# Performance work log

Measured on AMD Instinct MI355X. Metric: run time of the kernel, lower is better.

The kernel has to match this reference:

```python
import jax, jax.numpy as jnp
import numpy as np

EMBED_DIM = 1024
NUM_HEADS = 16
HEAD_DIM = EMBED_DIM // NUM_HEADS
HIDDEN_DIM = 4096
EPS = 1e-5


def setup_inputs() -> dict:
    key = jax.random.key(0)
    ks = jax.random.split(key, 12)
    B, N, C, H = 4, 2048, EMBED_DIM, HIDDEN_DIM
    s = 0.02
    return {
        "x": jax.random.normal(ks[0], (B, N, C), jnp.float32),
        "ln1_g": jnp.ones((C,), jnp.float32),
        "ln1_b": jnp.zeros((C,), jnp.float32),
        "w_qkv": jax.random.normal(ks[1], (C, 3 * C), jnp.float32) * s,
        "w_proj": jax.random.normal(ks[2], (C, C), jnp.float32) * s,
        "b_proj": jnp.zeros((C,), jnp.float32),
        "ln2_g": jnp.ones((C,), jnp.float32),
        "ln2_b": jnp.zeros((C,), jnp.float32),
        "w1": jax.random.normal(ks[3], (C, H), jnp.float32) * s,
        "b1": jnp.zeros((H,), jnp.float32),
        "w2": jax.random.normal(ks[4], (H, C), jnp.float32) * s,
        "b2": jnp.zeros((C,), jnp.float32),
    }


def _layernorm(x, g, b):
    mu = jnp.mean(x, axis=-1, keepdims=True)
    var = jnp.mean(jnp.square(x - mu), axis=-1, keepdims=True)
    return (x - mu) * jax.lax.rsqrt(var + EPS) * g + b


def reference(x, ln1_g, ln1_b, w_qkv, w_proj, b_proj, ln2_g, ln2_b, w1, b1, w2, b2):
    B, N, C = x.shape
    # --- attention sub-block ---
    h = _layernorm(x, ln1_g, ln1_b)
    qkv = h @ w_qkv  # [B,N,3C]
    qkv = qkv.reshape(B, N, 3, NUM_HEADS, HEAD_DIM).transpose(2, 0, 3, 1, 4)
    q, k, v = qkv[0], qkv[1], qkv[2]  # each [B,H,N,D]
    scale = HEAD_DIM ** -0.5
    attn = jnp.einsum("bhqd,bhkd->bhqk", q, k) * scale  # materialized scores
    attn = jax.nn.softmax(attn, axis=-1)
    o = jnp.einsum("bhqk,bhkd->bhqd", attn, v)
    o = o.transpose(0, 2, 1, 3).reshape(B, N, C)
    x = x + (o @ w_proj + b_proj)
    # --- MLP sub-block ---
    h = _layernorm(x, ln2_g, ln2_b)
    h = jax.nn.gelu(h @ w1 + b1, approximate=False)
    x = x + (h @ w2 + b2)
    return x
```

## Files before the change

kernel.cpp:

```cpp
#include <hip/hip_runtime.h>

#define B_    4
#define SEQ   2048
#define CDIM  1024
#define NHEAD 16
#define HDIM  64
#define HID   4096
#define MTOK  (B_*SEQ)

typedef unsigned short ushort_t;
typedef __bf16 bf16x8 __attribute__((ext_vector_type(8)));
typedef float  floatx4 __attribute__((ext_vector_type(4)));
typedef short  sh4     __attribute__((ext_vector_type(4)));

static __device__ __forceinline__ float us2f(ushort_t u) {
    union { unsigned u; float f; } z; z.u = ((unsigned)u) << 16; return z.f;
}
static __device__ __forceinline__ ushort_t f2b(float f) {
    union { __bf16 h; ushort_t u; } z; z.h = (__bf16)f; return z.u;
}

static __device__ __forceinline__ floatx4 mfma16(sh4 a, sh4 b, floatx4 c) {
#if __has_builtin(__builtin_amdgcn_mfma_f32_16x16x16bf16_1k)
    return __builtin_amdgcn_mfma_f32_16x16x16bf16_1k(a, b, c, 0, 0, 0);
#else
    asm("v_mfma_f32_16x16x16_bf16 %0, %1, %2, %0" : "+v"(c) : "v"(a), "v"(b));
    return c;
#endif
}

static __device__ __forceinline__ void gl_lds16(const ushort_t* g, ushort_t* l) {
    __builtin_amdgcn_global_load_lds(
        (const __attribute__((address_space(1))) void*)g,
        (__attribute__((address_space(3))) void*)l,
        16, 0, 0);
}

__global__ void k_detect(const unsigned* __restrict__ g1, int* __restrict__ flagp) {
    if (threadIdx.x == 0) flagp[0] = (g1[0] == 0x3F803F80u) ? 0 : 1;
}

__global__ __launch_bounds__(256) void k_cvt_params(const int* __restrict__ flagp,
        const void* s0, const void* s1, const void* s2, const void* s3,
        const void* s4, const void* s5, const void* s6,
        ushort_t* __restrict__ dst) {
    const int flag = *flagp;
    const int seg = blockIdx.y;
    const int i = blockIdx.x * 256 + threadIdx.x;
    const int sizes[7] = {1024, 1024, 1024, 1024, 1024, 4096, 1024};
    const int offs[7]  = {0, 1024, 2048, 3072, 4096, 5120, 9216};
    const void* sp = seg == 0 ? s0 : seg == 1 ? s1 : seg == 2 ? s2 :
                     seg == 3 ? s3 : seg == 4 ? s4 : seg == 5 ? s5 : s6;
    if (i < sizes[seg]) {
        float v = flag ? ((const float*)sp)[i] : us2f(((const ushort_t*)sp)[i]);
        dst[offs[seg] + i] = f2b(v);
    }
}

__global__ __launch_bounds__(256) void k_transpose_all(const int* __restrict__ flagp,
        const void* s_qkv, const void* s_proj, const void* s_w1, const void* s_w2,
        ushort_t* __restrict__ d_qkv, ushort_t* __restrict__ d_proj,
        ushort_t* __restrict__ d_w1, ushort_t* __restrict__ d_w2) {
    const int id = blockIdx.x;
    const void* src; ushort_t* dst; int R, C, tile;
    if (id < 3072)      { src = s_qkv;  dst = d_qkv;  R = 1024; C = 3072; tile = id; }
    else if (id < 4096) { src = s_proj; dst = d_proj; R = 1024; C = 1024; tile = id - 3072; }
    else if (id < 8192) { src = s_w1;   dst = d_w1;   R = 1024; C = 4096; tile = id - 4096; }
    else                { src = s_w2;   dst = d_w2;   R = 4096; C = 1024; tile = id - 8192; }
    const int ct = C >> 5;
    const int c0 = (tile % ct) * 32, r0 = (tile / ct) * 32;
    const int flag = *flagp;
    __shared__ ushort_t tl[32][33];
    const int tx = threadIdx.x & 31, ty = threadIdx.x >> 5;
    #pragma unroll
    for (int i = ty; i < 32; i += 8) {
        const size_t gi = (size_t)(r0 + i) * C + c0 + tx;
        tl[i][tx] = flag ? f2b(((const float*)src)[gi]) : ((const ushort_t*)src)[gi];
    }
    __syncthreads();
    #pragma unroll
    for (int i = ty; i < 32; i += 8)
        dst[(size_t)(c0 + i) * R + r0 + tx] = tl[tx][i];
}

template <int SRC>
__global__ __launch_bounds__(256) void k_layernorm(const int* __restrict__ flagp,
                                                   const float* __restrict__ xf,
                                                   const ushort_t* __restrict__ xb,
                                                   const ushort_t* __restrict__ gam,
                                                   const ushort_t* __restrict__ bet,
                                                   ushort_t* __restrict__ out) {
    const int row = blockIdx.x, t = threadIdx.x;
    const int lane = t & 63, wv = t >> 6;
    const size_t base = (size_t)row * CDIM + t * 4;
    float v[4];
    if (SRC == 1 || *flagp != 0) {
        float4 f = *(const float4*)(xf + base);
        v[0] = f.x; v[1] = f.y; v[2] = f.z; v[3] = f.w;
    } else {
        ushort4 u = *(const ushort4*)(xb + base);
        v[0] = us2f(u.x); v[1] = us2f(u.y); v[2] = us2f(u.z); v[3] = us2f(u.w);
    }
    float s = v[0] + v[1] + v[2] + v[3];
    float s2 = v[0]*v[0] + v[1]*v[1] + v[2]*v[2] + v[3]*v[3];
    #pragma unroll
    for (int m = 1; m < 64; m <<= 1) {
        s  += __shfl_xor(s,  m, 64);
        s2 += __shfl_xor(s2, m, 64);
    }
    __shared__ float redbuf[8];
    if (lane == 0) { redbuf[wv] = s; redbuf[4 + wv] = s2; }
    __syncthreads();
    s  = redbuf[0] + redbuf[1] + redbuf[2] + redbuf[3];
    s2 = redbuf[4] + redbuf[5] + redbuf[6] + redbuf[7];
    const float mu  = s * (1.0f / CDIM);
    const float var = s2 * (1.0f / CDIM) - mu * mu;
    const float rstd = rsqrtf(var + 1e-5f);
    const int cb = t * 4;
    ushort4 o;
    o.x = f2b((v[0] - mu) * rstd * us2f(gam[cb + 0]) + us2f(bet[cb + 0]));
    o.y = f2b((v[1] - mu) * rstd * us2f(gam[cb + 1]) + us2f(bet[cb + 1]));
    o.z = f2b((v[2] - mu) * rstd * us2f(gam[cb + 2]) + us2f(bet[cb + 2]));
    o.w = f2b((v[3] - mu) * rstd * us2f(gam[cb + 3]) + us2f(bet[cb + 3]));
    *(ushort4*)(out + base) = o;
}

enum { EPI_QKV = 0, EPI_BIAS_RES_F32 = 1, EPI_BIAS_GELU_BF16 = 2, EPI_FINAL = 3 };

template <int EPI, int KDIM>
__global__ __launch_bounds__(512, 2) void k_gemm2(const ushort_t* __restrict__ A,
                                                  const ushort_t* __restrict__ Bt,
                                                  const ushort_t* __restrict__ bias,
                                                  const float* __restrict__ resF,
                                                  const ushort_t* __restrict__ resU,
                                                  float* __restrict__ outF,
                                                  ushort_t* __restrict__ outB,
                                                  ushort_t* __restrict__ outV,
                                                  const int* __restrict__ flagp,
                                                  int N) {
    constexpr int NT = KDIM / 64;
    __shared__ ushort_t As[3][256 * 64];
    __shared__ ushort_t Bs[3][128 * 64];
    const int t = threadIdx.x, lane = t & 63, wv = t >> 6;
    const int quad = lane >> 4, cc = lane & 15;
    const int wm = wv >> 2, wn = wv & 3;
    const int m0 = blockIdx.y * 256, n0 = blockIdx.x * 128;

    auto stage = [&](int kt, int bf) {
        const int k0 = kt * 64;
        #pragma unroll
        for (int i = 0; i < 4; i++) {
            const int L = i * 512 + t;
            const int row = L >> 3;
            const int kc = (L & 7) ^ (row & 7);
            gl_lds16(A + (size_t)(m0 + row) * KDIM + k0 + kc * 8,
                     As[bf] + (size_t)(i * 512 + wv * 64) * 8);
        }
        #pragma unroll
        for (int i = 0; i < 2; i++) {
            const int L = i * 512 + t;
            const int row = L >> 3;
            const int kc = (L & 7) ^ (row & 7);
            gl_lds16(Bt + (size_t)(n0 + row) * KDIM + k0 + kc * 8,
                     Bs[bf] + (size_t)(i * 512 + wv * 64) * 8);
        }
    };

    floatx4 zv = {0.f, 0.f, 0.f, 0.f};
    floatx4 acc[8][2];
    #pragma unroll
    for (int m = 0; m < 8; m++) { acc[m][0] = zv; acc[m][1] = zv; }

    stage(0, 0); stage(1, 1); stage(2, 2);
    asm volatile("s_waitcnt vmcnt(12)" ::: "memory");
    __builtin_amdgcn_s_barrier();

    int bt = 0;
    for (int kt = 0; kt < NT; ++kt) {
        const ushort_t* pAs = As[bt];
        const ushort_t* pBs = Bs[bt];
        bf16x8 af[8][2], bfr[2][2];
        #pragma unroll
        for (int ks = 0; ks < 2; ks++) {
            const int sl = ((ks * 4 + quad) ^ (cc & 7)) * 8;
            #pragma unroll
            for (int m = 0; m < 8; m++)
                af[m][ks] = *(const bf16x8*)(pAs + (size_t)(wm * 128 + m * 16 + cc) * 64 + sl);
            #pragma unroll
            for (int n = 0; n < 2; n++)
                bfr[n][ks] = *(const bf16x8*)(pBs + (size_t)(wn * 32 + n * 16 + cc) * 64 + sl);
        }
        __builtin_amdgcn_s_setprio(1);
        #pragma unroll
        for (int m = 0; m < 8; m++)
            #pragma unroll
            for (int n = 0; n < 2; n++)
                acc[m][n] = __builtin_amdgcn_mfma_f32_16x16x32_bf16(
                    af[m][0], bfr[n][0], acc[m][n], 0, 0, 0);
        __builtin_amdgcn_s_setprio(0);
        asm volatile("s_waitcnt lgkmcnt(0)" ::: "memory");
        __builtin_amdgcn_s_barrier();
        if (kt + 3 < NT) stage(kt + 3, bt);
        __builtin_amdgcn_s_setprio(1);
        #pragma unroll
        for (int m = 0; m < 8; m++)
            #pragma unroll
            for (int n = 0; n < 2; n++)
                acc[m][n] = __builtin_amdgcn_mfma_f32_16x16x32_bf16(
                    af[m][1], bfr[n][1], acc[m][n], 0, 0, 0);
        __builtin_amdgcn_s_setprio(0);
        if (kt + 3 < NT)      asm volatile("s_waitcnt vmcnt(12)" ::: "memory");
        else if (kt + 2 < NT) asm volatile("s_waitcnt vmcnt(6)" ::: "memory");
        else if (kt + 1 < NT) asm volatile("s_waitcnt vmcnt(0)" ::: "memory");
        __builtin_amdgcn_s_barrier();
        bt = (bt == 2) ? 0 : bt + 1;
    }

    int flag = 0;
    if (EPI == EPI_BIAS_RES_F32 || EPI == EPI_FINAL) flag = *flagp;

    #pragma unroll
    for (int m = 0; m < 8; m++) {
        #pragma unroll
        for (int n = 0; n < 2; n++) {
            const int col = n0 + wn * 32 + n * 16 + cc;
            if (EPI == EPI_QKV) {
                if (col < 2048) {
                    const float sc = (col < 1024) ? 0.125f * 1.44269504f : 1.0f;
                    #pragma unroll
                    for (int i = 0; i < 4; i++) {
                        const int row = m0 + wm * 128 + m * 16 + quad * 4 + i;
                        outB[(size_t)row * 3072 + col] = f2b(acc[m][n][i] * sc);
                    }
                } else {
                    const int hh = (col - 2048) >> 6, d = (col - 2048) & 63;
                    const int r0w = m0 + wm * 128 + m * 16 + quad * 4;
                    const int bh = (r0w >> 11) * NHEAD + hh;
                    const int np = r0w & (SEQ - 1);
                    ushort4 pk;
                    pk.x = f2b(acc[m][n][0]);
                    pk.y = f2b(acc[m][n][1]);
                    pk.z = f2b(acc[m][n][2]);
                    pk.w = f2b(acc[m][n][3]);
                    *(ushort4*)(outV + ((size_t)bh * 64 + d) * SEQ + np) = pk;
                }
            } else {
                const float bv = us2f(bias[col]);
                #pragma unroll
                for (int i = 0; i < 4; i++) {
                    const int row = m0 + wm * 128 + m * 16 + quad * 4 + i;
                    const size_t idx = (size_t)row * N + col;
                    float v = acc[m][n][i] + bv;
                    if (EPI == EPI_BIAS_RES_F32) {
                        outF[idx] = v + (flag ? resF[idx] : us2f(resU[idx]));
                    } else if (EPI == EPI_BIAS_GELU_BF16) {
                        float u = v * v;
                        float w = -2.3022134f * v * __builtin_fmaf(0.044715f, u, 1.0f);
                        float e = __builtin_amdgcn_exp2f(fminf(w, 126.0f));
                        outB[idx] = f2b(v * __builtin_amdgcn_rcpf(1.0f + e));
                    } else {
                        float w = v + resF[idx];
                        if (flag != 0) outF[idx] = w;
                        else           outB[idx] = f2b(w);
                    }
                }
            }
        }
    }
}

__global__ __launch_bounds__(256) void k_attention(const ushort_t* __restrict__ qkv,
                                                   const ushort_t* __restrict__ vT,
                                                   ushort_t* __restrict__ o) {
    __shared__ ushort_t Kc[2][64 * 64];
    __shared__ ushort_t Vt[2][64 * 64];

    const int bh = blockIdx.x, qt = blockIdx.y;
    const int b = bh >> 4, h = bh & 15;
    const int t = threadIdx.x, lane = t & 63, wv = t >> 6;
    const int quad = lane >> 4, cc = lane & 15;
    const size_t rstr = 3 * CDIM;
    const ushort_t* Qb = qkv + (size_t)b * SEQ * rstr + h * HDIM;
    const ushort_t* Kb = Qb + CDIM;
    const ushort_t* Vb = vT + (size_t)bh * HDIM * SEQ;

    bf16x8 aq[2][2];
    #pragma unroll
    for (int mt = 0; mt < 2; mt++) {
        const int qrow = qt * 128 + wv * 32 + mt * 16 + cc;
        aq[mt][0] = *(const bf16x8*)(Qb + (size_t)qrow * rstr + quad * 8);
        aq[mt][1] = *(const bf16x8*)(Qb + (size_t)qrow * rstr + 32 + quad * 8);
    }

    floatx4 zv = {0.f, 0.f, 0.f, 0.f};
    floatx4 oacc[2][4];
    floatx4 lv[2];
    #pragma unroll
    for (int mt = 0; mt < 2; mt++) {
        lv[mt] = zv;
        #pragma unroll
        for (int dg = 0; dg < 4; dg++) oacc[mt][dg] = zv;
    }
    const sh4 ones4 = {0x3F80, 0x3F80, 0x3F80, 0x3F80};

    auto stage = [&](int c, int buf) {
        const int k0 = c * 64;
        #pragma unroll
        for (int ii = 0; ii < 2; ii++) {
            const int L = ii * 256 + t;
            const int r = L >> 3;
            const int kc = (L & 7) ^ (r & 7);
            gl_lds16(Kb + (size_t)(k0 + r) * rstr + kc * 8,
                     &Kc[buf][(size_t)(ii * 256 + wv * 64) * 8]);
            gl_lds16(Vb + (size_t)r * SEQ + k0 + kc * 8,
                     &Vt[buf][(size_t)(ii * 256 + wv * 64) * 8]);
        }
    };

    stage(0, 0);

    for (int c = 0; c < SEQ / 64; c++) {
        __syncthreads();
        if (c + 1 < SEQ / 64) stage(c + 1, (c + 1) & 1);
        const int bf = c & 1;

        floatx4 s[2][4];
        #pragma unroll
        for (int mt = 0; mt < 2; mt++)
            #pragma unroll
            for (int g = 0; g < 4; g++) s[mt][g] = zv;
        #pragma unroll
        for (int g = 0; g < 4; g++) {
            const ushort_t* kr = &Kc[bf][(size_t)(g * 16 + cc) * 64];
            bf16x8 bk0 = *(const bf16x8*)(kr + (quad ^ (cc & 7)) * 8);
            bf16x8 bk1 = *(const bf16x8*)(kr + ((4 + quad) ^ (cc & 7)) * 8);
            #pragma unroll
            for (int mt = 0; mt < 2; mt++) {
                s[mt][g] = __builtin_amdgcn_mfma_f32_16x16x32_bf16(bk0, aq[mt][0], s[mt][g], 0, 0, 0);
                s[mt][g] = __builtin_amdgcn_mfma_f32_16x16x32_bf16(bk1, aq[mt][1], s[mt][g], 0, 0, 0);
            }
        }

        sh4 pb[2][4];
        #pragma unroll
        for (int mt = 0; mt < 2; mt++)
            #pragma unroll
            for (int g = 0; g < 4; g++)
                #pragma unroll
                for (int i = 0; i < 4; i++) {
                    float p = __builtin_amdgcn_exp2f(s[mt][g][i]);
                    union { __bf16 h; short u; } cv; cv.h = (__bf16)p;
                    pb[mt][g][i] = cv.u;
                }

        #pragma unroll
        for (int kg = 0; kg < 4; kg++) {
            #pragma unroll
            for (int mt = 0; mt < 2; mt++)
                lv[mt] = mfma16(ones4, pb[mt][kg], lv[mt]);
            #pragma unroll
            for (int dg = 0; dg < 4; dg++) {
                const int d = dg * 16 + cc;
                const int ph = ((kg * 2 + (quad >> 1)) ^ (d & 7)) * 8 + (quad & 1) * 4;
                sh4 va = *(const sh4*)(&Vt[bf][(size_t)d * 64 + ph]);
                #pragma unroll
                for (int mt = 0; mt < 2; mt++)
                    oacc[mt][dg] = mfma16(va, pb[mt][kg], oacc[mt][dg]);
            }
        }
    }

    #pragma unroll
    for (int mt = 0; mt < 2; mt++) {
        const float rl = __builtin_amdgcn_rcpf(lv[mt][0]);
        const int tok = b * SEQ + qt * 128 + wv * 32 + mt * 16 + cc;
        #pragma unroll
        for (int dg = 0; dg < 4; dg++) {
            ushort4 pk;
            pk.x = f2b(oacc[mt][dg][0] * rl);
            pk.y = f2b(oacc[mt][dg][1] * rl);
            pk.z = f2b(oacc[mt][dg][2] * rl);
            pk.w = f2b(oacc[mt][dg][3] * rl);
            *(ushort4*)(o + (size_t)tok * CDIM + h * HDIM + dg * 16 + quad * 4) = pk;
        }
    }
}

extern "C" void kernel_launch(void* const* d_in, const int* in_sizes, int n_in,
                              void* d_out, int out_size, void* d_ws, size_t ws_size,
                              hipStream_t stream) {
    const void* x     = d_in[0];
    const void* ln1g  = d_in[1];
    const void* ln1b  = d_in[2];
    const void* wqkv  = d_in[3];
    const void* wproj = d_in[4];
    const void* bproj = d_in[5];
    const void* ln2g  = d_in[6];
    const void* ln2b  = d_in[7];
    const void* w1    = d_in[8];
    const void* b1    = d_in[9];
    const void* w2    = d_in[10];
    const void* b2    = d_in[11];

    char* ws = (char*)d_ws;
    size_t off = 0;
    auto alloc = [&](size_t bytes) {
        void* p = ws + off;
        off += (bytes + 255) & ~(size_t)255;
        return p;
    };
    int*      flagp  = (int*)alloc(256);
    ushort_t* params = (ushort_t*)alloc((size_t)10240 * 2);
    ushort_t* wqkvT  = (ushort_t*)alloc((size_t)3072 * 1024 * 2);
    ushort_t* wprojT = (ushort_t*)alloc((size_t)1024 * 1024 * 2);
    ushort_t* w1T    = (ushort_t*)alloc((size_t)4096 * 1024 * 2);
    ushort_t* w2T    = (ushort_t*)alloc((size_t)1024 * 4096 * 2);
    ushort_t* vTb    = (ushort_t*)alloc((size_t)MTOK * CDIM * 2);
    float*    x1     = (float*)alloc((size_t)MTOK * CDIM * 4);
    ushort_t* bufA   = (ushort_t*)alloc((size_t)MTOK * HID * 2);
    ushort_t* bufB   = (ushort_t*)alloc((size_t)MTOK * 3 * CDIM * 2);

    ushort_t* p_ln1g = params + 0;
    ushort_t* p_ln1b = params + 1024;
    ushort_t* p_ln2g = params + 2048;
    ushort_t* p_ln2b = params + 3072;
    ushort_t* p_bprj = params + 4096;
    ushort_t* p_b1   = params + 5120;
    ushort_t* p_b2   = params + 9216;

    ushort_t* h   = bufA;
    ushort_t* qkv = bufB;
    ushort_t* oo  = bufA;
    ushort_t* h2  = bufB;
    ushort_t* hh  = bufA;

    k_detect<<<1, 64, 0, stream>>>((const unsigned*)ln1g, flagp);
    k_cvt_params<<<dim3(16, 7), 256, 0, stream>>>(flagp,
        ln1g, ln1b, ln2g, ln2b, bproj, b1, b2, params);
    k_transpose_all<<<12288, 256, 0, stream>>>(flagp,
        wqkv, wproj, w1, w2, wqkvT, wprojT, w1T, w2T);

    k_layernorm<0><<<MTOK, 256, 0, stream>>>(flagp, (const float*)x, (const ushort_t*)x, p_ln1g, p_ln1b, h);
    k_gemm2<EPI_QKV, 1024><<<dim3(24, 32), 512, 0, stream>>>(
        h, wqkvT, nullptr, nullptr, nullptr, nullptr, qkv, vTb, flagp, 3072);
    k_attention<<<dim3(B_ * NHEAD, SEQ / 128), 256, 0, stream>>>(qkv, vTb, oo);
    k_gemm2<EPI_BIAS_RES_F32, 1024><<<dim3(8, 32), 512, 0, stream>>>(
        oo, wprojT, p_bprj, (const float*)x, (const ushort_t*)x, x1, nullptr, nullptr, flagp, 1024);
    k_layernorm<1><<<MTOK, 256, 0, stream>>>(flagp, x1, nullptr, p_ln2g, p_ln2b, h2);
    k_gemm2<EPI_BIAS_GELU_BF16, 1024><<<dim3(32, 32), 512, 0, stream>>>(
        h2, w1T, p_b1, nullptr, nullptr, nullptr, hh, nullptr, flagp, 4096);
    k_gemm2<EPI_FINAL, 4096><<<dim3(8, 32), 512, 0, stream>>>(
        hh, w2T, p_b2, x1, nullptr, (float*)d_out, (ushort_t*)d_out, nullptr, flagp, 1024);
}
```

Measured before the change: 564.2 us.

## Retile GEMMs to 256-wide N tiles with double buffering and split LDS fragment loads

Replaces the 256x128 triple-buffered GEMM with a templated kernel using 256-wide N tiles and a configurable M tile (256 for QKV/FC1, 128 for proj/FC2), double-buffered in LDS. Each warp now computes FMx4 fragments, which raises MFMA reuse per LDS load. The second-half K fragments are loaded after the first MFMA batch instead of up front, so LDS reads overlap with compute. Grids are resized to match. Double buffering leaves less prefetch depth, and the 128-row config yields 256 blocks, which may underfill the CUs.

```diff
diff --git a/kernel.cpp b/kernel.cpp
--- a/kernel.cpp
+++ b/kernel.cpp
@@ -127,8 +127,8 @@
 
 enum { EPI_QKV = 0, EPI_BIAS_RES_F32 = 1, EPI_BIAS_GELU_BF16 = 2, EPI_FINAL = 3 };
 
-template <int EPI, int KDIM>
-__global__ __launch_bounds__(512, 2) void k_gemm2(const ushort_t* __restrict__ A,
+template <int EPI, int KDIM, int FM>
+__global__ __launch_bounds__(512, 2) void k_gemm3(const ushort_t* __restrict__ A,
                                                   const ushort_t* __restrict__ Bt,
                                                   const ushort_t* __restrict__ bias,
                                                   const float* __restrict__ resF,
@@ -138,18 +138,20 @@
                                                   ushort_t* __restrict__ outV,
                                                   const int* __restrict__ flagp,
                                                   int N) {
+    constexpr int BM = FM * 32;
+    constexpr int AR = BM / 64;
     constexpr int NT = KDIM / 64;
-    __shared__ ushort_t As[3][256 * 64];
-    __shared__ ushort_t Bs[3][128 * 64];
+    __shared__ ushort_t As[2][BM * 64];
+    __shared__ ushort_t Bs[2][256 * 64];
     const int t = threadIdx.x, lane = t & 63, wv = t >> 6;
     const int quad = lane >> 4, cc = lane & 15;
     const int wm = wv >> 2, wn = wv & 3;
-    const int m0 = blockIdx.y * 256, n0 = blockIdx.x * 128;
+    const int m0 = blockIdx.y * BM, n0 = blockIdx.x * 256;
 
     auto stage = [&](int kt, int bf) {
         const int k0 = kt * 64;
         #pragma unroll
-        for (int i = 0; i < 4; i++) {
+        for (int i = 0; i < AR; i++) {
             const int L = i * 512 + t;
             const int row = L >> 3;
             const int kc = (L & 7) ^ (row & 7);
@@ -157,7 +159,7 @@
                      As[bf] + (size_t)(i * 512 + wv * 64) * 8);
         }
         #pragma unroll
-        for (int i = 0; i < 2; i++) {
+        for (int i = 0; i < 4; i++) {
             const int L = i * 512 + t;
             const int row = L >> 3;
             const int kc = (L & 7) ^ (row & 7);
@@ -167,74 +169,86 @@
     };
 
     floatx4 zv = {0.f, 0.f, 0.f, 0.f};
-    floatx4 acc[8][2];
-    #pragma unroll
-    for (int m = 0; m < 8; m++) { acc[m][0] = zv; acc[m][1] = zv; }
-
-    stage(0, 0); stage(1, 1); stage(2, 2);
-    asm volatile("s_waitcnt vmcnt(12)" ::: "memory");
+    floatx4 acc[FM][4];
+    #pragma unroll
+    for (int m = 0; m < FM; m++)
+        #pragma unroll
+        for (int n = 0; n < 4; n++) acc[m][n] = zv;
+
+    stage(0, 0); stage(1, 1);
+    if constexpr (FM == 8) asm volatile("s_waitcnt vmcnt(8)" ::: "memory");
+    else                   asm volatile("s_waitcnt vmcnt(6)" ::: "memory");
     __builtin_amdgcn_s_barrier();
 
-    int bt = 0;
+    int cur = 0;
     for (int kt = 0; kt < NT; ++kt) {
-        const ushort_t* pAs = As[bt];
-        const ushort_t* pBs = Bs[bt];
-        bf16x8 af[8][2], bfr[2][2];
-        #pragma unroll
-        for (int ks = 0; ks < 2; ks++) {
-            const int sl = ((ks * 4 + quad) ^ (cc & 7)) * 8;
-            #pragma unroll
-            for (int m = 0; m < 8; m++)
-                af[m][ks] = *(const bf16x8*)(pAs + (size_t)(wm * 128 + m * 16 + cc) * 64 + sl);
-            #pragma unroll
-            for (int n = 0; n < 2; n++)
-                bfr[n][ks] = *(const bf16x8*)(pBs + (size_t)(wn * 32 + n * 16 + cc) * 64 + sl);
-        }
+        const ushort_t* pAs = As[cur];
+        const ushort_t* pBs = Bs[cur];
+        bf16x8 af[FM], bfr[4];
+        const int sl0 = (quad ^ (cc & 7)) * 8;
+        #pragma unroll
+        for (int m = 0; m < FM; m++)
+            af[m] = *(const bf16x8*)(pAs + (size_t)(wm * (FM * 16) + m * 16 + cc) * 64 + sl0);
+        #pragma unroll
+        for (int n = 0; n < 4; n++)
+            bfr[n] = *(const bf16x8*)(pBs + (size_t)(wn * 64 + n * 16 + cc) * 64 + sl0);
         __builtin_amdgcn_s_setprio(1);
         #pragma unroll
-        for (int m = 0; m < 8; m++)
-            #pragma unroll
-            for (int n = 0; n < 2; n++)
+        for (int m = 0; m < FM; m++)
+            #pragma unroll
+            for (int n = 0; n < 4; n++)
                 acc[m][n] = __builtin_amdgcn_mfma_f32_16x16x32_bf16(
-                    af[m][0], bfr[n][0], acc[m][n], 0, 0, 0);
+                    af[m], bfr[n], acc[m][n], 0, 0, 0);
         __builtin_amdgcn_s_setprio(0);
+        bf16x8 ag[FM], bg[4];
+        const int sl1 = ((4 + quad) ^ (cc & 7)) * 8;
+        #pragma unroll
+        for (int m = 0; m < FM; m++)
+            ag[m] = *(const bf16x8*)(pAs + (size_t)(wm * (FM * 16) + m * 16 + cc) * 64 + sl1);
+        #pragma unroll
+        for (int n = 0; n < 4; n++)
+            bg[n] = *(const bf16x8*)(pBs + (size_t)(wn * 64 + n * 16 + cc) * 64 + sl1);
         asm volatile("s_waitcnt lgkmcnt(0)" ::: "memory");
+        __builtin_amdgcn_sched_barrier(0);
         __builtin_amdgcn_s_barrier();
-        if (kt + 3 < NT) stage(kt + 3, bt);
+        if (kt + 2 < NT) stage(kt + 2, cur);
         __builtin_amdgcn_s_setprio(1);
         #pragma unroll
-        for (int m = 0; m < 8; m++)
-            #pragma unroll
-            for (int n = 0; n < 2; n++)
+        for (int m = 0; m < FM; m++)
+            #pragma unroll
+            for (int n = 0; n < 4; n++)
                 acc[m][n] = __builtin_amdgcn_mfma_f32_16x16x32_bf16(
-                    af[m][1], bfr[n][1], acc[m][n], 0, 0, 0);
+                    ag[m], bg[n], acc[m][n], 0, 0, 0);
         __builtin_amdgcn_s_setprio(0);
-        if (kt + 3 < NT)      asm volatile("s_waitcnt vmcnt(12)" ::: "memory");
-        else if (kt + 2 < NT) asm volatile("s_waitcnt vmcnt(6)" ::: "memory");
-        else if (kt + 1 < NT) asm volatile("s_waitcnt vmcnt(0)" ::: "memory");
+        if (kt + 2 < NT) {
+            if constexpr (FM == 8) asm volatile("s_waitcnt vmcnt(8)" ::: "memory");
+            else                   asm volatile("s_waitcnt vmcnt(6)" ::: "memory");
+        } else if (kt + 1 < NT) {
+            asm volatile("s_waitcnt vmcnt(0)" ::: "memory");
+        }
         __builtin_amdgcn_s_barrier();
-        bt = (bt == 2) ? 0 : bt + 1;
+        cur ^= 1;
     }
 
     int flag = 0;
     if (EPI == EPI_BIAS_RES_F32 || EPI == EPI_FINAL) flag = *flagp;
 
     #pragma unroll
-    for (int m = 0; m < 8; m++) {
-        #pragma unroll
-        for (int n = 0; n < 2; n++) {
-            const int col = n0 + wn * 32 + n * 16 + cc;
+    for (int m = 0; m < FM; m++) {
+        #pragma unroll
+        for (int n = 0; n < 4; n++) {
+            const int col = n0 + wn * 64 + n * 16 + cc;
             if (EPI == EPI_QKV) {
                 if (col < 2048) {
                     const float sc = (col < 1024) ? 0.125f * 1.44269504f : 1.0f;
                     #pragma unroll
                     for (int i = 0; i < 4; i++) {
-                        const int row = m0 + wm * 128 + m * 16 + quad * 4 + i;
+                        const int row = m0 + wm * (FM * 16) + m * 16 + quad * 4 + i;
                         outB[(size_t)row * 3072 + col] = f2b(acc[m][n][i] * sc);
                     }
                 } else {
                     const int hh = (col - 2048) >> 6, d = (col - 2048) & 63;
-                    const int r0w = m0 + wm * 128 + m * 16 + quad * 4;
+                    const int r0w = m0 + wm * (FM * 16) + m * 16 + quad * 4;
                     const int bh = (r0w >> 11) * NHEAD + hh;
                     const int np = r0w & (SEQ - 1);
                     ushort4 pk;
@@ -248,7 +262,7 @@
                 const float bv = us2f(bias[col]);
                 #pragma unroll
                 for (int i = 0; i < 4; i++) {
-                    const int row = m0 + wm * 128 + m * 16 + quad * 4 + i;
+                    const int row = m0 + wm * (FM * 16) + m * 16 + quad * 4 + i;
                     const size_t idx = (size_t)row * N + col;
                     float v = acc[m][n][i] + bv;
                     if (EPI == EPI_BIAS_RES_F32) {
@@ -441,14 +455,14 @@
         wqkv, wproj, w1, w2, wqkvT, wprojT, w1T, w2T);
 
     k_layernorm<0><<<MTOK, 256, 0, stream>>>(flagp, (const float*)x, (const ushort_t*)x, p_ln1g, p_ln1b, h);
-    k_gemm2<EPI_QKV, 1024><<<dim3(24, 32), 512, 0, stream>>>(
+    k_gemm3<EPI_QKV, 1024, 8><<<dim3(12, 32), 512, 0, stream>>>(
         h, wqkvT, nullptr, nullptr, nullptr, nullptr, qkv, vTb, flagp, 3072);
     k_attention<<<dim3(B_ * NHEAD, SEQ / 128), 256, 0, stream>>>(qkv, vTb, oo);
-    k_gemm2<EPI_BIAS_RES_F32, 1024><<<dim3(8, 32), 512, 0, stream>>>(
+    k_gemm3<EPI_BIAS_RES_F32, 1024, 4><<<dim3(4, 64), 512, 0, stream>>>(
         oo, wprojT, p_bprj, (const float*)x, (const ushort_t*)x, x1, nullptr, nullptr, flagp, 1024);
     k_layernorm<1><<<MTOK, 256, 0, stream>>>(flagp, x1, nullptr, p_ln2g, p_ln2b, h2);
-    k_gemm2<EPI_BIAS_GELU_BF16, 1024><<<dim3(32, 32), 512, 0, stream>>>(
+    k_gemm3<EPI_BIAS_GELU_BF16, 1024, 8><<<dim3(16, 32), 512, 0, stream>>>(
         h2, w1T, p_b1, nullptr, nullptr, nullptr, hh, nullptr, flagp, 4096);
-    k_gemm2<EPI_FINAL, 4096><<<dim3(8, 32), 512, 0, stream>>>(
+    k_gemm3<EPI_FINAL, 4096, 4><<<dim3(4, 64), 512, 0, stream>>>(
         hh, w2T, p_b2, x1, nullptr, (float*)d_out, (ushort_t*)d_out, nullptr, flagp, 1024);
 }
```

After: 534.7 us. 1.06x faster.

## Rewrite GEMM as templated 256-wide N tile with interleaved fragment loads

Applied to the files above, without the earlier changes.

Replaces the 256x128 GEMM tile with a templated BMx256 tile (BM 128 or 256), with double or triple buffering chosen by BM. The main loop is split into four phases that interleave LDS fragment loads with MFMA groups and issue the next global prefetch earlier, aiming to overlap LDS reads with matrix math. Each GEMM launch gets a new grid shape and BM choice. The extra barriers per k-step and the fewer blocks for the smaller GEMMs may cost synchronization overhead or reduce occupancy.

```diff
diff --git a/kernel.cpp b/kernel.cpp
--- a/kernel.cpp
+++ b/kernel.cpp
@@ -127,8 +127,8 @@
 
 enum { EPI_QKV = 0, EPI_BIAS_RES_F32 = 1, EPI_BIAS_GELU_BF16 = 2, EPI_FINAL = 3 };
 
-template <int EPI, int KDIM>
-__global__ __launch_bounds__(512, 2) void k_gemm2(const ushort_t* __restrict__ A,
+template <int EPI, int KDIM, int BM>
+__global__ __launch_bounds__(512, 2) void k_gemm4(const ushort_t* __restrict__ A,
                                                   const ushort_t* __restrict__ Bt,
                                                   const ushort_t* __restrict__ bias,
                                                   const float* __restrict__ resF,
@@ -138,103 +138,150 @@
                                                   ushort_t* __restrict__ outV,
                                                   const int* __restrict__ flagp,
                                                   int N) {
-    constexpr int NT = KDIM / 64;
-    __shared__ ushort_t As[3][256 * 64];
-    __shared__ ushort_t Bs[3][128 * 64];
+    constexpr int WR   = BM / 2;
+    constexpr int FR   = WR / 16;
+    constexpr int ART  = (BM * 64) / 4096;
+    constexpr int NT   = KDIM / 64;
+    constexpr int NBUF = (BM == 128) ? 3 : 2;
+    constexpr int LA   = NBUF - 1;
+    __shared__ ushort_t As[NBUF][BM * 64];
+    __shared__ ushort_t Bs[NBUF][256 * 64];
     const int t = threadIdx.x, lane = t & 63, wv = t >> 6;
     const int quad = lane >> 4, cc = lane & 15;
     const int wm = wv >> 2, wn = wv & 3;
-    const int m0 = blockIdx.y * 256, n0 = blockIdx.x * 128;
-
-    auto stage = [&](int kt, int bf) {
-        const int k0 = kt * 64;
-        #pragma unroll
-        for (int i = 0; i < 4; i++) {
-            const int L = i * 512 + t;
-            const int row = L >> 3;
-            const int kc = (L & 7) ^ (row & 7);
-            gl_lds16(A + (size_t)(m0 + row) * KDIM + k0 + kc * 8,
-                     As[bf] + (size_t)(i * 512 + wv * 64) * 8);
-        }
-        #pragma unroll
-        for (int i = 0; i < 2; i++) {
-            const int L = i * 512 + t;
-            const int row = L >> 3;
-            const int kc = (L & 7) ^ (row & 7);
-            gl_lds16(Bt + (size_t)(n0 + row) * KDIM + k0 + kc * 8,
-                     Bs[bf] + (size_t)(i * 512 + wv * 64) * 8);
+    const int m0 = blockIdx.y * BM, n0 = blockIdx.x * 256;
+
+    const int rl = lane >> 3, kc = (lane & 7) ^ (rl & 7);
+    auto stage_tile = [&](int kt, int d) {
+        #pragma unroll
+        for (int r = 0; r < ART; ++r) {
+            const int row = r * 64 + wv * 8 + rl;
+            gl_lds16(A + (size_t)(m0 + row) * KDIM + kt * 64 + kc * 8,
+                     As[d] + r * 4096 + wv * 512);
+        }
+        #pragma unroll
+        for (int r = 0; r < 4; ++r) {
+            const int row = r * 64 + wv * 8 + rl;
+            gl_lds16(Bt + (size_t)(n0 + row) * KDIM + kt * 64 + kc * 8,
+                     Bs[d] + r * 4096 + wv * 512);
         }
     };
 
     floatx4 zv = {0.f, 0.f, 0.f, 0.f};
-    floatx4 acc[8][2];
-    #pragma unroll
-    for (int m = 0; m < 8; m++) { acc[m][0] = zv; acc[m][1] = zv; }
-
-    stage(0, 0); stage(1, 1); stage(2, 2);
-    asm volatile("s_waitcnt vmcnt(12)" ::: "memory");
+    floatx4 acc[FR][4];
+    #pragma unroll
+    for (int m = 0; m < FR; m++)
+        #pragma unroll
+        for (int n = 0; n < 4; n++) acc[m][n] = zv;
+
+    #pragma unroll
+    for (int l = 0; l < LA; ++l) stage_tile(l, l);
+    if constexpr (NBUF == 3) asm volatile("s_waitcnt vmcnt(6)" ::: "memory");
+    else                     asm volatile("s_waitcnt vmcnt(0)" ::: "memory");
     __builtin_amdgcn_s_barrier();
 
-    int bt = 0;
+    int cur = 0;
     for (int kt = 0; kt < NT; ++kt) {
-        const ushort_t* pAs = As[bt];
-        const ushort_t* pBs = Bs[bt];
-        bf16x8 af[8][2], bfr[2][2];
-        #pragma unroll
-        for (int ks = 0; ks < 2; ks++) {
-            const int sl = ((ks * 4 + quad) ^ (cc & 7)) * 8;
-            #pragma unroll
-            for (int m = 0; m < 8; m++)
-                af[m][ks] = *(const bf16x8*)(pAs + (size_t)(wm * 128 + m * 16 + cc) * 64 + sl);
-            #pragma unroll
-            for (int n = 0; n < 2; n++)
-                bfr[n][ks] = *(const bf16x8*)(pBs + (size_t)(wn * 32 + n * 16 + cc) * 64 + sl);
-        }
+        const ushort_t* pA = As[cur];
+        const ushort_t* pB = Bs[cur];
+        const int sl0 = (quad ^ (cc & 7)) * 8;
+        const int sl1 = ((4 + quad) ^ (cc & 7)) * 8;
+        bf16x8 af[FR], bfr[2];
+
+        #pragma unroll
+        for (int m = 0; m < FR; m++)
+            af[m] = *(const bf16x8*)(pA + (size_t)(wm * WR + m * 16 + cc) * 64 + sl0);
+        #pragma unroll
+        for (int n = 0; n < 2; n++)
+            bfr[n] = *(const bf16x8*)(pB + (size_t)(wn * 64 + n * 16 + cc) * 64 + sl0);
+        if (kt + LA < NT) {
+            int d = cur + LA; if (d >= NBUF) d -= NBUF;
+            stage_tile(kt + LA, d);
+        }
+        __builtin_amdgcn_s_barrier();
+        asm volatile("s_waitcnt lgkmcnt(0)" ::: "memory");
         __builtin_amdgcn_s_setprio(1);
         #pragma unroll
-        for (int m = 0; m < 8; m++)
-            #pragma unroll
-            for (int n = 0; n < 2; n++)
-                acc[m][n] = __builtin_amdgcn_mfma_f32_16x16x32_bf16(
-                    af[m][0], bfr[n][0], acc[m][n], 0, 0, 0);
+        for (int m = 0; m < FR; m++) {
+            acc[m][0] = __builtin_amdgcn_mfma_f32_16x16x32_bf16(af[m], bfr[0], acc[m][0], 0, 0, 0);
+            acc[m][1] = __builtin_amdgcn_mfma_f32_16x16x32_bf16(af[m], bfr[1], acc[m][1], 0, 0, 0);
+        }
         __builtin_amdgcn_s_setprio(0);
+        __builtin_amdgcn_s_barrier();
+
+        bf16x8 bg[2];
+        #pragma unroll
+        for (int n = 0; n < 2; n++)
+            bg[n] = *(const bf16x8*)(pB + (size_t)(wn * 64 + (2 + n) * 16 + cc) * 64 + sl0);
+        __builtin_amdgcn_s_barrier();
         asm volatile("s_waitcnt lgkmcnt(0)" ::: "memory");
-        __builtin_amdgcn_s_barrier();
-        if (kt + 3 < NT) stage(kt + 3, bt);
         __builtin_amdgcn_s_setprio(1);
         #pragma unroll
-        for (int m = 0; m < 8; m++)
-            #pragma unroll
-            for (int n = 0; n < 2; n++)
-                acc[m][n] = __builtin_amdgcn_mfma_f32_16x16x32_bf16(
-                    af[m][1], bfr[n][1], acc[m][n], 0, 0, 0);
+        for (int m = 0; m < FR; m++) {
+            acc[m][2] = __builtin_amdgcn_mfma_f32_16x16x32_bf16(af[m], bg[0], acc[m][2], 0, 0, 0);
+            acc[m][3] = __builtin_amdgcn_mfma_f32_16x16x32_bf16(af[m], bg[1], acc[m][3], 0, 0, 0);
+        }
         __builtin_amdgcn_s_setprio(0);
-        if (kt + 3 < NT)      asm volatile("s_waitcnt vmcnt(12)" ::: "memory");
-        else if (kt + 2 < NT) asm volatile("s_waitcnt vmcnt(6)" ::: "memory");
-        else if (kt + 1 < NT) asm volatile("s_waitcnt vmcnt(0)" ::: "memory");
-        __builtin_amdgcn_s_barrier();
-        bt = (bt == 2) ? 0 : bt + 1;
+        __builtin_amdgcn_s_barrier();
+
+        #pragma unroll
+        for (int m = 0; m < FR; m++)
+            af[m] = *(const bf16x8*)(pA + (size_t)(wm * WR + m * 16 + cc) * 64 + sl1);
+        #pragma unroll
+        for (int n = 0; n < 2; n++)
+            bfr[n] = *(const bf16x8*)(pB + (size_t)(wn * 64 + n * 16 + cc) * 64 + sl1);
+        __builtin_amdgcn_s_barrier();
+        asm volatile("s_waitcnt lgkmcnt(0)" ::: "memory");
+        __builtin_amdgcn_s_setprio(1);
+        #pragma unroll
+        for (int m = 0; m < FR; m++) {
+            acc[m][0] = __builtin_amdgcn_mfma_f32_16x16x32_bf16(af[m], bfr[0], acc[m][0], 0, 0, 0);
+            acc[m][1] = __builtin_amdgcn_mfma_f32_16x16x32_bf16(af[m], bfr[1], acc[m][1], 0, 0, 0);
+        }
+        __builtin_amdgcn_s_setprio(0);
+        __builtin_amdgcn_s_barrier();
+
+        #pragma unroll
+        for (int n = 0; n < 2; n++)
+            bg[n] = *(const bf16x8*)(pB + (size_t)(wn * 64 + (2 + n) * 16 + cc) * 64 + sl1);
+        __builtin_amdgcn_s_barrier();
+        asm volatile("s_waitcnt lgkmcnt(0)" ::: "memory");
+        __builtin_amdgcn_s_setprio(1);
+        #pragma unroll
+        for (int m = 0; m < FR; m++) {
+            acc[m][2] = __builtin_amdgcn_mfma_f32_16x16x32_bf16(af[m], bg[0], acc[m][2], 0, 0, 0);
+            acc[m][3] = __builtin_amdgcn_mfma_f32_16x16x32_bf16(af[m], bg[1], acc[m][3], 0, 0, 0);
+        }
+        __builtin_amdgcn_s_setprio(0);
+        if constexpr (NBUF == 3) {
+            if (kt + 2 < NT)      asm volatile("s_waitcnt vmcnt(6)" ::: "memory");
+            else if (kt + 1 < NT) asm volatile("s_waitcnt vmcnt(0)" ::: "memory");
+        } else {
+            if (kt + 1 < NT)      asm volatile("s_waitcnt vmcnt(0)" ::: "memory");
+        }
+        __builtin_amdgcn_s_barrier();
+        cur = (cur + 1 == NBUF) ? 0 : cur + 1;
     }
 
     int flag = 0;
     if (EPI == EPI_BIAS_RES_F32 || EPI == EPI_FINAL) flag = *flagp;
 
     #pragma unroll
-    for (int m = 0; m < 8; m++) {
-        #pragma unroll
-        for (int n = 0; n < 2; n++) {
-            const int col = n0 + wn * 32 + n * 16 + cc;
+    for (int m = 0; m < FR; m++) {
+        #pragma unroll
+        for (int n = 0; n < 4; n++) {
+            const int col = n0 + wn * 64 + n * 16 + cc;
             if (EPI == EPI_QKV) {
                 if (col < 2048) {
                     const float sc = (col < 1024) ? 0.125f * 1.44269504f : 1.0f;
                     #pragma unroll
                     for (int i = 0; i < 4; i++) {
-                        const int row = m0 + wm * 128 + m * 16 + quad * 4 + i;
+                        const int row = m0 + wm * WR + m * 16 + quad * 4 + i;
                         outB[(size_t)row * 3072 + col] = f2b(acc[m][n][i] * sc);
                     }
                 } else {
                     const int hh = (col - 2048) >> 6, d = (col - 2048) & 63;
-                    const int r0w = m0 + wm * 128 + m * 16 + quad * 4;
+                    const int r0w = m0 + wm * WR + m * 16 + quad * 4;
                     const int bh = (r0w >> 11) * NHEAD + hh;
                     const int np = r0w & (SEQ - 1);
                     ushort4 pk;
@@ -248,7 +295,7 @@
                 const float bv = us2f(bias[col]);
                 #pragma unroll
                 for (int i = 0; i < 4; i++) {
-                    const int row = m0 + wm * 128 + m * 16 + quad * 4 + i;
+                    const int row = m0 + wm * WR + m * 16 + quad * 4 + i;
                     const size_t idx = (size_t)row * N + col;
                     float v = acc[m][n][i] + bv;
                     if (EPI == EPI_BIAS_RES_F32) {
@@ -372,15 +419,15 @@
 
     #pragma unroll
     for (int mt = 0; mt < 2; mt++) {
-        const float rl = __builtin_amdgcn_rcpf(lv[mt][0]);
+        const float rl2 = __builtin_amdgcn_rcpf(lv[mt][0]);
         const int tok = b * SEQ + qt * 128 + wv * 32 + mt * 16 + cc;
         #pragma unroll
         for (int dg = 0; dg < 4; dg++) {
             ushort4 pk;
-            pk.x = f2b(oacc[mt][dg][0] * rl);
-            pk.y = f2b(oacc[mt][dg][1] * rl);
-            pk.z = f2b(oacc[mt][dg][2] * rl);
-            pk.w = f2b(oacc[mt][dg][3] * rl);
+            pk.x = f2b(oacc[mt][dg][0] * rl2);
+            pk.y = f2b(oacc[mt][dg][1] * rl2);
+            pk.z = f2b(oacc[mt][dg][2] * rl2);
+            pk.w = f2b(oacc[mt][dg][3] * rl2);
             *(ushort4*)(o + (size_t)tok * CDIM + h * HDIM + dg * 16 + quad * 4) = pk;
         }
     }
@@ -441,14 +488,14 @@
         wqkv, wproj, w1, w2, wqkvT, wprojT, w1T, w2T);
 
     k_layernorm<0><<<MTOK, 256, 0, stream>>>(flagp, (const float*)x, (const ushort_t*)x, p_ln1g, p_ln1b, h);
-    k_gemm2<EPI_QKV, 1024><<<dim3(24, 32), 512, 0, stream>>>(
+    k_gemm4<EPI_QKV, 1024, 128><<<dim3(12, 64), 512, 0, stream>>>(
         h, wqkvT, nullptr, nullptr, nullptr, nullptr, qkv, vTb, flagp, 3072);
     k_attention<<<dim3(B_ * NHEAD, SEQ / 128), 256, 0, stream>>>(qkv, vTb, oo);
-    k_gemm2<EPI_BIAS_RES_F32, 1024><<<dim3(8, 32), 512, 0, stream>>>(
+    k_gemm4<EPI_BIAS_RES_F32, 1024, 128><<<dim3(4, 64), 512, 0, stream>>>(
         oo, wprojT, p_bprj, (const float*)x, (const ushort_t*)x, x1, nullptr, nullptr, flagp, 1024);
     k_layernorm<1><<<MTOK, 256, 0, stream>>>(flagp, x1, nullptr, p_ln2g, p_ln2b, h2);
-    k_gemm2<EPI_BIAS_GELU_BF16, 1024><<<dim3(32, 32), 512, 0, stream>>>(
+    k_gemm4<EPI_BIAS_GELU_BF16, 1024, 256><<<dim3(16, 32), 512, 0, stream>>>(
         h2, w1T, p_b1, nullptr, nullptr, nullptr, hh, nullptr, flagp, 4096);
-    k_gemm2<EPI_FINAL, 4096><<<dim3(8, 32), 512, 0, stream>>>(
+    k_gemm4<EPI_FINAL, 4096, 128><<<dim3(4, 64), 512, 0, stream>>>(
         hh, w2T, p_b2, x1, nullptr, (float*)d_out, (ushort_t*)d_out, nullptr, flagp, 1024);
 }
```

New measurement: 575.9 us. 2.1% more time.
